# Optimization experiments

Measured on AMD Instinct MI355X. Metric: run time of the kernel, lower is better.

Reference implementation:

```python
import jax, jax.numpy as jnp
import numpy as np
import math

# Config (matches init_kwargs): ProphetNet-style ngram self-attention
T, B, E, H, NGRAM, NB, MAXD = 512, 4, 1024, 16, 2, 32, 128
HD = E // H
TGT = (1 + NGRAM) * T
NEG = -1e9


def _buckets(rel):
    # faithful numpy version of _relative_positions_bucket (bidirectional=False)
    n = np.maximum(-rel, 0)
    max_exact = NB // 2
    is_small = n < max_exact
    large = max_exact + np.log(np.maximum(n, 1) / max_exact) / math.log(MAXD / max_exact) * (NB - max_exact)
    large = np.minimum(large, NB - 1).astype(np.int32)
    return np.where(is_small, n.astype(np.int32), large)


def setup_inputs() -> dict:
    key = jax.random.key(0)
    ks = jax.random.split(key, 4)
    s = 0.02
    # position ids 1..T (ProphetNet positions start at 1); precompute bucket tables
    pos = np.arange(1, T + 1, dtype=np.int64)[None, :].repeat(B, axis=0)          # [B,T]
    main_rel = pos[:, None, :] - pos[:, :, None]                                  # [B,T,T]
    pred_keys = np.concatenate([pos - 1, pos], axis=-1)                           # [B,2T]
    pred_rel = pred_keys[:, None, :] - pos[:, :, None]                            # [B,T,2T]
    return {
        "query": jax.random.normal(ks[0], (TGT, B, E), jnp.float32),
        "in_proj_weight": jax.random.normal(ks[1], (3 * E, E), jnp.float32) * s,
        "in_proj_bias": jnp.zeros((3 * E,), jnp.float32),
        "rel_w": jax.random.normal(ks[2], (NB * H, E), jnp.float32) * s,
        "rel_b": jnp.zeros((NB * H,), jnp.float32),
        "out_w": jax.random.normal(ks[3], (E, E), jnp.float32) * s,
        "out_b": jnp.zeros((E,), jnp.float32),
        "main_buckets": jnp.asarray(_buckets(main_rel), jnp.int32),
        "predict_buckets": jnp.asarray(_buckets(pred_rel), jnp.int32),
    }


def reference(query, in_proj_weight, in_proj_bias, rel_w, rel_b, out_w, out_b,
              main_buckets, predict_buckets):
    scaling = HD ** -0.5
    qkv = query @ in_proj_weight.T + in_proj_bias                  # [TGT,B,3E]
    q, k, v = jnp.split(qkv, 3, axis=-1)
    q = q * scaling

    def heads(x):  # [TGT,B,E] -> [B*H, TGT, HD]
        return x.reshape(TGT, B * H, HD).transpose(1, 0, 2)

    q, k, v = heads(q), heads(k), heads(v)
    q_main, k_main, v_main = q[:, :T], k[:, :T], v[:, :T]

    def ngram_split(x):  # [B*H, NGRAM*T, HD] -> [N, B*H, T, HD]
        return x[:, T:].reshape(B * H, NGRAM, T, HD).transpose(1, 0, 2, 3)

    q_pred, k_pred, v_pred = ngram_split(q), ngram_split(k), ngram_split(v)
    h_main = query[:T]                                             # [T,B,E]
    h_pred = query[T:].reshape(NGRAM, T, B, E)

    # ---------- main stream ----------
    aw_main = jnp.einsum('bth,bsh->bts', q_main, k_main)           # [B*H,T,T]
    vals = h_main.transpose(1, 0, 2) @ rel_w.T + rel_b             # [B,T,NB*H]
    vals = vals.reshape(B, T, NB, H).transpose(0, 3, 1, 2)         # [B,H,T,NB]
    idx = jnp.broadcast_to(main_buckets[:, None], (B, H, T, T))
    rel_main = jnp.take_along_axis(vals, idx, axis=-1).reshape(B * H, T, T)
    causal = jnp.triu(jnp.full((T, T), NEG, jnp.float32), 1)       # self_attn_mask
    aw_main = jax.nn.softmax(aw_main + rel_main + causal[None], axis=-1)
    attn_main = jnp.einsum('bts,bsh->bth', aw_main, v_main)        # [B*H,T,HD]
    attn_main = attn_main.transpose(1, 0, 2).reshape(1, T, B, E)
    attn_main = attn_main @ out_w.T + out_b

    # ---------- ngram predict streams ----------
    k_ng = jnp.concatenate([jnp.broadcast_to(k_main[None], (NGRAM, B * H, T, HD)), k_pred], axis=2)
    v_ng = jnp.concatenate([jnp.broadcast_to(v_main[None], (NGRAM, B * H, T, HD)), v_pred], axis=2)
    aw_ng = jnp.einsum('nbtc,nbsc->nbts', q_pred, k_ng)            # [N,B*H,T,2T]
    valsn = h_pred.transpose(0, 2, 1, 3) @ rel_w.T + rel_b         # [N,B,T,NB*H]
    valsn = valsn.reshape(NGRAM, B, T, NB, H).transpose(0, 1, 4, 2, 3)  # [N,B,H,T,NB]
    idxn = jnp.broadcast_to(predict_buckets[None, :, None], (NGRAM, B, H, T, 2 * T))
    rel_ng = jnp.take_along_axis(valsn, idxn, axis=-1).reshape(NGRAM, B * H, T, 2 * T)
    # ngram_mask: main part causal, predict part only the matching position
    ng_mask = jnp.concatenate([causal, NEG * (1.0 - jnp.eye(T, dtype=jnp.float32))], axis=1)  # [T,2T]
    aw_ng = jax.nn.softmax(aw_ng + rel_ng + ng_mask[None, None], axis=-1)
    attn_ng = jnp.einsum('nbts,nbsc->nbtc', aw_ng, v_ng)           # [N,B*H,T,HD]
    attn_ng = attn_ng.transpose(0, 2, 1, 3).reshape(NGRAM, T, B, E)
    attn_ng = attn_ng @ out_w.T + out_b

    return jnp.concatenate([attn_main, attn_ng], axis=0).reshape(TGT, B, E)
```

## Files before the change

kernel.cpp:

```cpp
#include <hip/hip_runtime.h>
#include <hip/hip_bf16.h>
#include <math.h>

constexpr int T_ = 512;
constexpr int B_ = 4;
constexpr int E_ = 1024;
constexpr int H_ = 16;
constexpr int NGRAM_ = 2;
constexpr int TGT_ = (1 + NGRAM_) * T_;
constexpr int ROWS_ = TGT_ * B_;

typedef __bf16 bf16_t;
typedef __bf16 bf16x8 __attribute__((ext_vector_type(8)));
typedef __bf16 bf16x4 __attribute__((ext_vector_type(4)));
typedef float f32x4 __attribute__((ext_vector_type(4)));

#define GLL(gaddr, laddr)                                                     \
  __builtin_amdgcn_global_load_lds(                                           \
      (const __attribute__((address_space(1))) void*)(gaddr),                 \
      (__attribute__((address_space(3))) void*)(laddr), 16, 0, 0)

#define BARX()  asm volatile("s_barrier" ::: "memory")
#define WVM7()  asm volatile("s_waitcnt vmcnt(7)" ::: "memory")
#define WVM0()  asm volatile("s_waitcnt vmcnt(0)" ::: "memory")

__global__ __launch_bounds__(256) void prep(
    const float* __restrict__ query, const float* __restrict__ ipw,
    const float* __restrict__ relw, const float* __restrict__ outw,
    bf16_t* __restrict__ qb, bf16_t* __restrict__ ipwb,
    bf16_t* __restrict__ relwb, bf16_t* __restrict__ outwb) {
  const int i = blockIdx.x * 256 + threadIdx.x;
  constexpr int N1 = ROWS_ * E_ / 4;
  constexpr int N2 = 3 * E_ * E_ / 4;
  constexpr int N3 = 512 * E_ / 4;
  constexpr int N4 = E_ * E_ / 4;
  const float4* src;
  bf16_t* dst;
  int j = i;
  if (i < N1) { src = (const float4*)query; dst = qb; }
  else if (i < N1 + N2) { src = (const float4*)ipw; dst = ipwb; j = i - N1; }
  else if (i < N1 + N2 + N3) { src = (const float4*)relw; dst = relwb; j = i - N1 - N2; }
  else if (i < N1 + N2 + N3 + N4) { src = (const float4*)outw; dst = outwb; j = i - N1 - N2 - N3; }
  else return;
  const float4 v = src[j];
  bf16x4 o;
  o[0] = (bf16_t)v.x; o[1] = (bf16_t)v.y;
  o[2] = (bf16_t)v.z; o[3] = (bf16_t)v.w;
  ((bf16x4*)dst)[j] = o;
}

__device__ __forceinline__ int sw256(int row, int col) {
  return row * 256 + ((((col >> 3) ^ (row & 31)) << 3) | (col & 7));
}

__global__ __launch_bounds__(512, 2) void bgemm_proj(
    const bf16_t* __restrict__ A, const bf16_t* __restrict__ W,
    const float* __restrict__ ipb, const float* __restrict__ relb,
    bf16_t* __restrict__ qkvb, float* __restrict__ relv2,
    bf16_t* __restrict__ vT) {
  __shared__ bf16_t smem[57344];
  bf16_t* As0 = smem;
  bf16_t* As1 = smem + 12288;
  bf16_t* Bs0 = smem + 24576;
  bf16_t* Bs1 = smem + 24576 + 16384;

  const int tid = threadIdx.x;
  const int wave = tid >> 6, lane = tid & 63;
  const int wr = wave >> 2, wc = wave & 3;
  const int pid = blockIdx.y * 14 + blockIdx.x;
  const int lid = (pid & 7) * 56 + (pid >> 3);
  const int by = lid / 14;
  const int bx = lid - by * 14;
  const int bm = by * 192, bn = bx * 256;
  const int q = lane >> 4, ln = lane & 15;
  const int grow = tid >> 3;
  const int gcol = ((tid & 7) ^ (grow & 7)) * 8;
  const int co[2] = {((q) ^ (ln & 7)) * 8, ((4 + q) ^ (ln & 7)) * 8};

  f32x4 acc[6][4];
#pragma unroll
  for (int mi = 0; mi < 6; ++mi)
#pragma unroll
    for (int ni = 0; ni < 4; ++ni)
#pragma unroll
      for (int r = 0; r < 4; ++r) acc[mi][ni][r] = 0.f;

  auto stage = [&](int kt, bf16_t* la, bf16_t* lb) {
    const int kc = kt * 64 + gcol;
#pragma unroll
    for (int p = 0; p < 3; ++p)
      GLL(&A[(size_t)(bm + p * 64 + grow) * 1024 + kc], &la[p * 4096 + tid * 8]);
#pragma unroll
    for (int p = 0; p < 4; ++p)
      GLL(&W[(size_t)(bn + p * 64 + grow) * 1024 + kc], &lb[p * 4096 + tid * 8]);
  };

  auto compute_tile = [&](const bf16_t* la, const bf16_t* lb) {
    bf16x8 a0[3], a1[3], b0[4], b1[4];
#pragma unroll
    for (int ni = 0; ni < 4; ++ni)
      b0[ni] = *(const bf16x8*)&lb[(wc * 64 + ni * 16 + ln) * 64 + co[0]];
#pragma unroll
    for (int mi = 0; mi < 3; ++mi)
      a0[mi] = *(const bf16x8*)&la[(wr * 96 + mi * 16 + ln) * 64 + co[0]];
#pragma unroll
    for (int mi = 0; mi < 3; ++mi)
      a1[mi] = *(const bf16x8*)&la[(wr * 96 + (3 + mi) * 16 + ln) * 64 + co[0]];
    __builtin_amdgcn_s_setprio(1);
#pragma unroll
    for (int mi = 0; mi < 3; ++mi)
#pragma unroll
      for (int ni = 0; ni < 4; ++ni)
        acc[mi][ni] = __builtin_amdgcn_mfma_f32_16x16x32_bf16(
            a0[mi], b0[ni], acc[mi][ni], 0, 0, 0);
    __builtin_amdgcn_s_setprio(0);
#pragma unroll
    for (int ni = 0; ni < 4; ++ni)
      b1[ni] = *(const bf16x8*)&lb[(wc * 64 + ni * 16 + ln) * 64 + co[1]];
#pragma unroll
    for (int mi = 0; mi < 3; ++mi)
      a0[mi] = *(const bf16x8*)&la[(wr * 96 + mi * 16 + ln) * 64 + co[1]];
    __builtin_amdgcn_s_setprio(1);
#pragma unroll
    for (int mi = 0; mi < 3; ++mi)
#pragma unroll
      for (int ni = 0; ni < 4; ++ni)
        acc[3 + mi][ni] = __builtin_amdgcn_mfma_f32_16x16x32_bf16(
            a1[mi], b0[ni], acc[3 + mi][ni], 0, 0, 0);
    __builtin_amdgcn_s_setprio(0);
#pragma unroll
    for (int mi = 0; mi < 3; ++mi)
      a1[mi] = *(const bf16x8*)&la[(wr * 96 + (3 + mi) * 16 + ln) * 64 + co[1]];
    __builtin_amdgcn_s_setprio(1);
#pragma unroll
    for (int mi = 0; mi < 3; ++mi)
#pragma unroll
      for (int ni = 0; ni < 4; ++ni)
        acc[mi][ni] = __builtin_amdgcn_mfma_f32_16x16x32_bf16(
            a0[mi], b1[ni], acc[mi][ni], 0, 0, 0);
    __builtin_amdgcn_s_setprio(0);
    __builtin_amdgcn_s_setprio(1);
#pragma unroll
    for (int mi = 0; mi < 3; ++mi)
#pragma unroll
      for (int ni = 0; ni < 4; ++ni)
        acc[3 + mi][ni] = __builtin_amdgcn_mfma_f32_16x16x32_bf16(
            a1[mi], b1[ni], acc[3 + mi][ni], 0, 0, 0);
    __builtin_amdgcn_s_setprio(0);
  };

  stage(0, As0, Bs0);
  stage(1, As1, Bs1);

  for (int kt = 0; kt < 16; kt += 2) {
    WVM7(); BARX();
    compute_tile(As0, Bs0);
    BARX();
    if (kt + 2 < 16) stage(kt + 2, As0, Bs0);
    if (kt < 14) { WVM7(); } else { WVM0(); }
    BARX();
    compute_tile(As1, Bs1);
    BARX();
    if (kt + 3 < 16) stage(kt + 3, As1, Bs1);
  }

  if (bn < 2048) {
    const float sc = (bn < 1024) ? 0.125f : 1.0f;
#pragma unroll
    for (int mi = 0; mi < 6; ++mi) {
#pragma unroll
      for (int ni = 0; ni < 4; ++ni) {
        const int col = bn + wc * 64 + ni * 16 + ln;
        const float bv = ipb[col];
#pragma unroll
        for (int r = 0; r < 4; ++r) {
          const int row = bm + wr * 96 + mi * 16 + q * 4 + r;
          qkvb[(size_t)row * 3072 + col] = (bf16_t)((acc[mi][ni][r] + bv) * sc);
        }
      }
    }
  } else if (bn < 3072) {
    __syncthreads();
#pragma unroll
    for (int mi = 0; mi < 6; ++mi) {
#pragma unroll
      for (int ni = 0; ni < 4; ++ni) {
        const int col_l = wc * 64 + ni * 16 + ln;
        const float bv = ipb[bn + col_l];
#pragma unroll
        for (int r = 0; r < 4; ++r) {
          const int row_l = wr * 96 + mi * 16 + q * 4 + r;
          smem[sw256(row_l, col_l)] = (bf16_t)(acc[mi][ni][r] + bv);
        }
      }
    }
    __syncthreads();
    const int h0 = (bn - 2048) >> 6;
    const int tb0 = bm >> 2;
#pragma unroll
    for (int e = 0; e < 2; ++e) {
      const int task = e * 512 + tid;
      const int b = task & 3;
      const int c = task >> 2;
      const int h = h0 + (c >> 6);
      const int d = c & 63;
      const size_t base = ((size_t)((b * 16 + h) * 64 + d)) * (size_t)TGT_ + tb0;
#pragma unroll
      for (int k = 0; k < 6; ++k) {
        bf16x8 v8;
#pragma unroll
        for (int i = 0; i < 8; ++i)
          v8[i] = smem[sw256((k * 8 + i) * 4 + b, c)];
        *(bf16x8*)&vT[base + k * 8] = v8;
      }
    }
  } else {
    const int cb = bn - 3072 + wc * 64;
    float4 rb4;
#pragma unroll
    for (int ni = 0; ni < 4; ++ni)
      ((float*)&rb4)[ni] = relb[cb + ni * 16 + ln];
    const int bkbase = cb >> 4;
#pragma unroll
    for (int mi = 0; mi < 6; ++mi) {
#pragma unroll
      for (int r = 0; r < 4; ++r) {
        const int row = bm + wr * 96 + mi * 16 + q * 4 + r;
        float4 v;
        v.x = acc[mi][0][r] + rb4.x;
        v.y = acc[mi][1][r] + rb4.y;
        v.z = acc[mi][2][r] + rb4.z;
        v.w = acc[mi][3][r] + rb4.w;
        *(float4*)&relv2[(size_t)row * 512 + ln * 32 + bkbase] = v;
      }
    }
  }
}

__global__ __launch_bounds__(256, 4) void bgemm_out(
    const bf16_t* __restrict__ A, const bf16_t* __restrict__ W,
    const float* __restrict__ bias, float* __restrict__ C, int N) {
  __shared__ bf16_t As[128 * 64];
  __shared__ bf16_t Bs[128 * 64];

  const int tid = threadIdx.x;
  const int wave = tid >> 6, lane = tid & 63;
  const int wr = wave >> 1, wc = wave & 1;
  const int pid = blockIdx.y * 8 + blockIdx.x;
  const int lid = (pid & 7) * 48 + (pid >> 3);
  const int bm = (lid >> 3) * 128, bn = (lid & 7) * 128;
  const int q = lane >> 4, ln = lane & 15;
  const int grow = tid >> 3;
  const int gcol = ((tid & 7) ^ (grow & 7)) * 8;

  f32x4 acc[4][4];
#pragma unroll
  for (int mi = 0; mi < 4; ++mi)
#pragma unroll
    for (int ni = 0; ni < 4; ++ni)
#pragma unroll
      for (int r = 0; r < 4; ++r) acc[mi][ni][r] = 0.f;

  const int co[2] = {((q) ^ (ln & 7)) * 8, ((4 + q) ^ (ln & 7)) * 8};

  for (int k0 = 0; k0 < 1024; k0 += 64) {
    __syncthreads();
#pragma unroll
    for (int p = 0; p < 4; ++p) {
      GLL(&A[(size_t)(bm + p * 32 + grow) * 1024 + k0 + gcol], &As[p * 2048 + tid * 8]);
      GLL(&W[(size_t)(bn + p * 32 + grow) * 1024 + k0 + gcol], &Bs[p * 2048 + tid * 8]);
    }
    __syncthreads();
#pragma unroll
    for (int t = 0; t < 2; ++t) {
      bf16x8 af[4], bf[4];
#pragma unroll
      for (int mi = 0; mi < 4; ++mi)
        af[mi] = *(const bf16x8*)&As[(wr * 64 + mi * 16 + ln) * 64 + co[t]];
#pragma unroll
      for (int ni = 0; ni < 4; ++ni)
        bf[ni] = *(const bf16x8*)&Bs[(wc * 64 + ni * 16 + ln) * 64 + co[t]];
#pragma unroll
      for (int mi = 0; mi < 4; ++mi)
#pragma unroll
        for (int ni = 0; ni < 4; ++ni)
          acc[mi][ni] = __builtin_amdgcn_mfma_f32_16x16x32_bf16(
              af[mi], bf[ni], acc[mi][ni], 0, 0, 0);
    }
  }

#pragma unroll
  for (int mi = 0; mi < 4; ++mi) {
#pragma unroll
    for (int ni = 0; ni < 4; ++ni) {
      const int col = bn + wc * 64 + ni * 16 + ln;
      const float bv = bias[col];
#pragma unroll
      for (int r = 0; r < 4; ++r) {
        const int row = bm + wr * 64 + mi * 16 + q * 4 + r;
        C[(size_t)row * N + col] = acc[mi][ni][r] + bv;
      }
    }
  }
}

__device__ __forceinline__ int bucket_of(int n) {
  if (n < 16) return n;
  const float lf = __log2f((float)n);
  int b = (int)(16.0f + (lf - 4.0f) * 5.3333333f);
  return b > 31 ? 31 : b;
}

__global__ __launch_bounds__(256, 2) void flash_mfma(
    const bf16_t* __restrict__ qkvb, const bf16_t* __restrict__ vT,
    const float* __restrict__ relv2, bf16_t* __restrict__ attn) {
  __shared__ bf16_t Ks[2][64 * 64];
  __shared__ bf16_t Vts[2][64 * 64];
  __shared__ bf16_t Ps[4][16 * 64];
  __shared__ bf16_t biasS[3][64 * 33];

  const int bh = blockIdx.x;
  const int qt = 7 - ((blockIdx.y + (bh >> 3)) & 7);
  const int tq0 = qt * 64;
  const int b = bh >> 4, h = bh & 15;
  const int tid = threadIdx.x;
  const int wave = tid >> 6, lane = tid & 63;
  const int q = lane >> 4, ln = lane & 15;
  const int m0 = wave * 16;
  const int grow = tid >> 3;
  const int gcol = ((tid & 7) ^ (grow & 7)) * 8;
  const int co[2] = {((q) ^ (ln & 7)) * 8, ((4 + q) ^ (ln & 7)) * 8};

#pragma unroll
  for (int z = 0; z < 3; ++z) {
#pragma unroll
    for (int u = 0; u < 2; ++u) {
      const int c = u * 256 + tid;
      const int row = c >> 3, j4 = (c & 7) * 4;
      const float4 v = *(const float4*)
          &relv2[((size_t)(z * T_ + tq0 + row) * B_ + b) * 512 + h * 32 + j4];
      biasS[z][row * 33 + j4 + 0] = (bf16_t)v.x;
      biasS[z][row * 33 + j4 + 1] = (bf16_t)v.y;
      biasS[z][row * 33 + j4 + 2] = (bf16_t)v.z;
      biasS[z][row * 33 + j4 + 3] = (bf16_t)v.w;
    }
  }

#pragma unroll
  for (int u = 0; u < 2; ++u) {
    const int sr = u * 32 + grow;
    GLL(&qkvb[((size_t)(0 * T_ + tq0 + sr) * B_ + b) * 3072 + h * 64 + gcol],
        &Ks[0][u * 2048 + tid * 8]);
    GLL(&qkvb[((size_t)(1 * T_ + tq0 + sr) * B_ + b) * 3072 + h * 64 + gcol],
        &Vts[0][u * 2048 + tid * 8]);
    GLL(&qkvb[((size_t)(2 * T_ + tq0 + sr) * B_ + b) * 3072 + h * 64 + gcol],
        &Ks[1][u * 2048 + tid * 8]);
  }
  __syncthreads();

  bf16x8 aq[3][2];
  aq[0][0] = *(const bf16x8*)&Ks[0][(m0 + ln) * 64 + co[0]];
  aq[0][1] = *(const bf16x8*)&Ks[0][(m0 + ln) * 64 + co[1]];
  aq[1][0] = *(const bf16x8*)&Vts[0][(m0 + ln) * 64 + co[0]];
  aq[1][1] = *(const bf16x8*)&Vts[0][(m0 + ln) * 64 + co[1]];
  aq[2][0] = *(const bf16x8*)&Ks[1][(m0 + ln) * 64 + co[0]];
  aq[2][1] = *(const bf16x8*)&Ks[1][(m0 + ln) * 64 + co[1]];

  float bv31[3][4], bv0[3][4];
#pragma unroll
  for (int z = 0; z < 3; ++z)
#pragma unroll
    for (int r = 0; r < 4; ++r) {
      const int rloc = m0 + q * 4 + r;
      bv31[z][r] = (float)biasS[z][rloc * 33 + 31];
      bv0[z][r] = (float)biasS[z][rloc * 33];
    }

  f32x4 Od[3][4];
  float lpart[3][4];
#pragma unroll
  for (int z = 0; z < 3; ++z)
#pragma unroll
    for (int r = 0; r < 4; ++r) {
      lpart[z][r] = 0.f;
#pragma unroll
      for (int tc = 0; tc < 4; ++tc) Od[z][tc][r] = 0.f;
    }

  const int ntiles = qt + 3;

  auto stage_tile = [&](int jj, int buf) {
    const int krb = (jj <= qt) ? jj * 64 : ((jj - qt) * T_ + tq0);
#pragma unroll
    for (int u = 0; u < 2; ++u) {
      const int sr = u * 32 + grow;
      GLL(&qkvb[((size_t)(krb + sr) * B_ + b) * 3072 + 1024 + h * 64 + gcol],
          &Ks[buf][u * 2048 + tid * 8]);
      GLL(&vT[((size_t)bh * 64 + sr) * (size_t)TGT_ + krb + gcol],
          &Vts[buf][u * 2048 + tid * 8]);
    }
  };

  __syncthreads();
  stage_tile(0, 0);
  __syncthreads();

  for (int jj = 0; jj < ntiles; ++jj) {
    const int cur = jj & 1;
    if (jj + 1 < ntiles) stage_tile(jj + 1, cur ^ 1);

    const int krb = (jj <= qt) ? jj * 64 : ((jj - qt) * T_ + tq0);

    bf16x8 kf[4][2], vf[4][2];
#pragma unroll
    for (int tc = 0; tc < 4; ++tc) {
      kf[tc][0] = *(const bf16x8*)&Ks[cur][(tc * 16 + ln) * 64 + co[0]];
      kf[tc][1] = *(const bf16x8*)&Ks[cur][(tc * 16 + ln) * 64 + co[1]];
      vf[tc][0] = *(const bf16x8*)&Vts[cur][(tc * 16 + ln) * 64 + co[0]];
      vf[tc][1] = *(const bf16x8*)&Vts[cur][(tc * 16 + ln) * 64 + co[1]];
    }

    if (jj <= qt) {
      const bool far = (jj <= qt - 3);
#pragma unroll
      for (int z = 0; z < 3; ++z) {
        f32x4 acc[4];
#pragma unroll
        for (int tc = 0; tc < 4; ++tc)
#pragma unroll
          for (int r = 0; r < 4; ++r) acc[tc][r] = 0.f;
#pragma unroll
        for (int tc = 0; tc < 4; ++tc) {
          acc[tc] = __builtin_amdgcn_mfma_f32_16x16x32_bf16(aq[z][0], kf[tc][0], acc[tc], 0, 0, 0);
          acc[tc] = __builtin_amdgcn_mfma_f32_16x16x32_bf16(aq[z][1], kf[tc][1], acc[tc], 0, 0, 0);
        }

        if (far) {
#pragma unroll
          for (int r = 0; r < 4; ++r) {
            const float bv = bv31[z][r];
#pragma unroll
            for (int tc = 0; tc < 4; ++tc) {
              const float p = __expf(acc[tc][r] + bv);
              lpart[z][r] += p;
              const int pc = (tc * 2 + (ln >> 3)) ^ ((q * 4 + r) & 7);
              Ps[wave][(q * 4 + r) * 64 + pc * 8 + (ln & 7)] = (bf16_t)p;
            }
          }
        } else {
#pragma unroll
          for (int r = 0; r < 4; ++r) {
            const int rloc = m0 + q * 4 + r;
            const int dbase = tq0 + rloc - krb;
#pragma unroll
            for (int tc = 0; tc < 4; ++tc) {
              const int sl = tc * 16 + ln;
              const int d = dbase - sl;
              const bool valid = (jj < qt) | (d >= 0);
              int n = d < 0 ? 0 : d;
              if (z > 0) n += 1;
              const float bv = (float)biasS[z][rloc * 33 + bucket_of(n)];
              const float p = valid ? __expf(acc[tc][r] + bv) : 0.f;
              lpart[z][r] += p;
              const int pc = (tc * 2 + (ln >> 3)) ^ ((q * 4 + r) & 7);
              Ps[wave][(q * 4 + r) * 64 + pc * 8 + (ln & 7)] = (bf16_t)p;
            }
          }
        }

        bf16x8 ap[2];
        ap[0] = *(const bf16x8*)&Ps[wave][ln * 64 + co[0]];
        ap[1] = *(const bf16x8*)&Ps[wave][ln * 64 + co[1]];
#pragma unroll
        for (int tc = 0; tc < 4; ++tc) {
          Od[z][tc] = __builtin_amdgcn_mfma_f32_16x16x32_bf16(ap[0], vf[tc][0], Od[z][tc], 0, 0, 0);
          Od[z][tc] = __builtin_amdgcn_mfma_f32_16x16x32_bf16(ap[1], vf[tc][1], Od[z][tc], 0, 0, 0);
        }
      }
    } else {
#pragma unroll
      for (int z = 1; z <= 2; ++z) {
        if (jj - qt == z) {
          f32x4 acc[4];
#pragma unroll
          for (int tc = 0; tc < 4; ++tc)
#pragma unroll
            for (int r = 0; r < 4; ++r) acc[tc][r] = 0.f;
#pragma unroll
          for (int tc = 0; tc < 4; ++tc) {
            acc[tc] = __builtin_amdgcn_mfma_f32_16x16x32_bf16(aq[z][0], kf[tc][0], acc[tc], 0, 0, 0);
            acc[tc] = __builtin_amdgcn_mfma_f32_16x16x32_bf16(aq[z][1], kf[tc][1], acc[tc], 0, 0, 0);
          }
#pragma unroll
          for (int r = 0; r < 4; ++r) {
            const int rloc = m0 + q * 4 + r;
            const float bv = bv0[z][r];
#pragma unroll
            for (int tc = 0; tc < 4; ++tc) {
              const int sl = tc * 16 + ln;
              const float p = (sl == rloc) ? __expf(acc[tc][r] + bv) : 0.f;
              lpart[z][r] += p;
              const int pc = (tc * 2 + (ln >> 3)) ^ ((q * 4 + r) & 7);
              Ps[wave][(q * 4 + r) * 64 + pc * 8 + (ln & 7)] = (bf16_t)p;
            }
          }
          bf16x8 ap[2];
          ap[0] = *(const bf16x8*)&Ps[wave][ln * 64 + co[0]];
          ap[1] = *(const bf16x8*)&Ps[wave][ln * 64 + co[1]];
#pragma unroll
          for (int tc = 0; tc < 4; ++tc) {
            Od[z][tc] = __builtin_amdgcn_mfma_f32_16x16x32_bf16(ap[0], vf[tc][0], Od[z][tc], 0, 0, 0);
            Od[z][tc] = __builtin_amdgcn_mfma_f32_16x16x32_bf16(ap[1], vf[tc][1], Od[z][tc], 0, 0, 0);
          }
        }
      }
    }
    __syncthreads();
  }

#pragma unroll
  for (int z = 0; z < 3; ++z) {
#pragma unroll
    for (int r = 0; r < 4; ++r) {
      float l = lpart[z][r];
      l += __shfl_xor(l, 1, 16);
      l += __shfl_xor(l, 2, 16);
      l += __shfl_xor(l, 4, 16);
      l += __shfl_xor(l, 8, 16);
      const float inv = 1.f / l;
      const size_t rowbase =
          ((size_t)(z * T_ + tq0 + m0 + q * 4 + r) * B_ + b) * (size_t)E_ + h * 64;
#pragma unroll
      for (int tc = 0; tc < 4; ++tc)
        attn[rowbase + tc * 16 + ln] = (bf16_t)(Od[z][tc][r] * inv);
    }
  }
}

extern "C" void kernel_launch(void* const* d_in, const int* in_sizes, int n_in,
                              void* d_out, int out_size, void* d_ws, size_t ws_size,
                              hipStream_t stream) {
  const float* query = (const float*)d_in[0];
  const float* ipw   = (const float*)d_in[1];
  const float* ipb   = (const float*)d_in[2];
  const float* relw  = (const float*)d_in[3];
  const float* relb  = (const float*)d_in[4];
  const float* outw  = (const float*)d_in[5];
  const float* outb  = (const float*)d_in[6];
  float* out = (float*)d_out;

  bf16_t* qkvb  = (bf16_t*)d_ws;
  float*  relv2 = (float*)(qkvb + (size_t)ROWS_ * 3 * E_);
  bf16_t* qb    = (bf16_t*)(relv2 + (size_t)ROWS_ * 512);
  bf16_t* ipwb  = qb + (size_t)ROWS_ * E_;
  bf16_t* relwb = ipwb + (size_t)(3 * E_) * E_;
  bf16_t* outwb = relwb + (size_t)512 * E_;
  bf16_t* attnb = outwb + (size_t)E_ * E_;
  bf16_t* vT    = attnb + (size_t)ROWS_ * E_;

  const dim3 blk(256);

  {
    const int ntot = (ROWS_ * E_ + 3 * E_ * E_ + 512 * E_ + E_ * E_) / 4;
    prep<<<dim3((ntot + 255) / 256), blk, 0, stream>>>(
        query, ipw, relw, outw, qb, ipwb, relwb, outwb);
  }

  bgemm_proj<<<dim3(3584 / 256, ROWS_ / 192), dim3(512), 0, stream>>>(
      qb, ipwb, ipb, relb, qkvb, relv2, vT);

  flash_mfma<<<dim3(64, 8), blk, 0, stream>>>(
      qkvb, vT, relv2, attnb);

  bgemm_out<<<dim3(E_ / 128, ROWS_ / 128), blk, 0, stream>>>(
      attnb, outwb, outb, out, E_);
}
```

Measured before the change: 239.6 us.

## Double-buffer output GEMM with 192x128 tiles and split projection GEMM launch

```diff
diff --git a/kernel.cpp b/kernel.cpp
--- a/kernel.cpp
+++ b/kernel.cpp
@@ -20,9 +20,10 @@
       (const __attribute__((address_space(1))) void*)(gaddr),                 \
       (__attribute__((address_space(3))) void*)(laddr), 16, 0, 0)
 
-#define BARX()  asm volatile("s_barrier" ::: "memory")
-#define WVM7()  asm volatile("s_waitcnt vmcnt(7)" ::: "memory")
-#define WVM0()  asm volatile("s_waitcnt vmcnt(0)" ::: "memory")
+#define BARX()   asm volatile("s_barrier" ::: "memory")
+#define WVM7()   asm volatile("s_waitcnt vmcnt(7)" ::: "memory")
+#define WVM10()  asm volatile("s_waitcnt vmcnt(10)" ::: "memory")
+#define WVM0()   asm volatile("s_waitcnt vmcnt(0)" ::: "memory")
 
 __global__ __launch_bounds__(256) void prep(
     const float* __restrict__ query, const float* __restrict__ ipw,
@@ -57,7 +58,7 @@
     const bf16_t* __restrict__ A, const bf16_t* __restrict__ W,
     const float* __restrict__ ipb, const float* __restrict__ relb,
     bf16_t* __restrict__ qkvb, float* __restrict__ relv2,
-    bf16_t* __restrict__ vT) {
+    bf16_t* __restrict__ vT, int bn0) {
   __shared__ bf16_t smem[57344];
   bf16_t* As0 = smem;
   bf16_t* As1 = smem + 12288;
@@ -67,11 +68,13 @@
   const int tid = threadIdx.x;
   const int wave = tid >> 6, lane = tid & 63;
   const int wr = wave >> 2, wc = wave & 3;
-  const int pid = blockIdx.y * 14 + blockIdx.x;
-  const int lid = (pid & 7) * 56 + (pid >> 3);
-  const int by = lid / 14;
-  const int bx = lid - by * 14;
-  const int bm = by * 192, bn = bx * 256;
+  const int nx = gridDim.x;
+  const int pid = blockIdx.y * nx + blockIdx.x;
+  const int chunk = (nx * gridDim.y) >> 3;
+  const int lid = (pid & 7) * chunk + (pid >> 3);
+  const int by = lid / nx;
+  const int bx = lid - by * nx;
+  const int bm = by * 192, bn = bn0 + bx * 256;
   const int q = lane >> 4, ln = lane & 15;
   const int grow = tid >> 3;
   const int gcol = ((tid & 7) ^ (grow & 7)) * 8;
@@ -237,68 +240,123 @@
   }
 }
 
-__global__ __launch_bounds__(256, 4) void bgemm_out(
+__global__ __launch_bounds__(256, 1) void bgemm_out(
     const bf16_t* __restrict__ A, const bf16_t* __restrict__ W,
-    const float* __restrict__ bias, float* __restrict__ C, int N) {
-  __shared__ bf16_t As[128 * 64];
-  __shared__ bf16_t Bs[128 * 64];
+    const float* __restrict__ bias, float* __restrict__ C) {
+  __shared__ bf16_t smem[40960];
 
   const int tid = threadIdx.x;
   const int wave = tid >> 6, lane = tid & 63;
   const int wr = wave >> 1, wc = wave & 1;
   const int pid = blockIdx.y * 8 + blockIdx.x;
-  const int lid = (pid & 7) * 48 + (pid >> 3);
-  const int bm = (lid >> 3) * 128, bn = (lid & 7) * 128;
+  const int lid = (pid & 7) * 32 + (pid >> 3);
+  const int bm = (lid >> 3) * 192, bn = (lid & 7) * 128;
   const int q = lane >> 4, ln = lane & 15;
   const int grow = tid >> 3;
   const int gcol = ((tid & 7) ^ (grow & 7)) * 8;
-
-  f32x4 acc[4][4];
-#pragma unroll
-  for (int mi = 0; mi < 4; ++mi)
+  const int co[2] = {((q) ^ (ln & 7)) * 8, ((4 + q) ^ (ln & 7)) * 8};
+
+  f32x4 acc[6][4];
+#pragma unroll
+  for (int mi = 0; mi < 6; ++mi)
 #pragma unroll
     for (int ni = 0; ni < 4; ++ni)
 #pragma unroll
       for (int r = 0; r < 4; ++r) acc[mi][ni][r] = 0.f;
 
-  const int co[2] = {((q) ^ (ln & 7)) * 8, ((4 + q) ^ (ln & 7)) * 8};
-
-  for (int k0 = 0; k0 < 1024; k0 += 64) {
-    __syncthreads();
-#pragma unroll
-    for (int p = 0; p < 4; ++p) {
-      GLL(&A[(size_t)(bm + p * 32 + grow) * 1024 + k0 + gcol], &As[p * 2048 + tid * 8]);
-      GLL(&W[(size_t)(bn + p * 32 + grow) * 1024 + k0 + gcol], &Bs[p * 2048 + tid * 8]);
-    }
-    __syncthreads();
-#pragma unroll
-    for (int t = 0; t < 2; ++t) {
-      bf16x8 af[4], bf[4];
-#pragma unroll
-      for (int mi = 0; mi < 4; ++mi)
-        af[mi] = *(const bf16x8*)&As[(wr * 64 + mi * 16 + ln) * 64 + co[t]];
-#pragma unroll
-      for (int ni = 0; ni < 4; ++ni)
-        bf[ni] = *(const bf16x8*)&Bs[(wc * 64 + ni * 16 + ln) * 64 + co[t]];
-#pragma unroll
-      for (int mi = 0; mi < 4; ++mi)
-#pragma unroll
-        for (int ni = 0; ni < 4; ++ni)
-          acc[mi][ni] = __builtin_amdgcn_mfma_f32_16x16x32_bf16(
-              af[mi], bf[ni], acc[mi][ni], 0, 0, 0);
-    }
-  }
-
-#pragma unroll
-  for (int mi = 0; mi < 4; ++mi) {
+  auto stage = [&](int kt) {
+    bf16_t* s = smem + (kt & 1) * 20480;
+    const int kc = kt * 64 + gcol;
+#pragma unroll
+    for (int p = 0; p < 6; ++p)
+      GLL(&A[(size_t)(bm + p * 32 + grow) * 1024 + kc], &s[p * 2048 + tid * 8]);
+#pragma unroll
+    for (int p = 0; p < 4; ++p)
+      GLL(&W[(size_t)(bn + p * 32 + grow) * 1024 + kc],
+          &s[12288 + p * 2048 + tid * 8]);
+  };
+
+  auto compute_tile = [&](int kt) {
+    const bf16_t* la = smem + (kt & 1) * 20480;
+    const bf16_t* lb = la + 12288;
+    bf16x8 a0[3], a1[3], b0[4], b1[4];
+#pragma unroll
+    for (int ni = 0; ni < 4; ++ni)
+      b0[ni] = *(const bf16x8*)&lb[(wc * 64 + ni * 16 + ln) * 64 + co[0]];
+#pragma unroll
+    for (int mi = 0; mi < 3; ++mi)
+      a0[mi] = *(const bf16x8*)&la[(wr * 96 + mi * 16 + ln) * 64 + co[0]];
+#pragma unroll
+    for (int mi = 0; mi < 3; ++mi)
+      a1[mi] = *(const bf16x8*)&la[(wr * 96 + (3 + mi) * 16 + ln) * 64 + co[0]];
+    __builtin_amdgcn_s_setprio(1);
+#pragma unroll
+    for (int mi = 0; mi < 3; ++mi)
+#pragma unroll
+      for (int ni = 0; ni < 4; ++ni)
+        acc[mi][ni] = __builtin_amdgcn_mfma_f32_16x16x32_bf16(
+            a0[mi], b0[ni], acc[mi][ni], 0, 0, 0);
+    __builtin_amdgcn_s_setprio(0);
+#pragma unroll
+    for (int ni = 0; ni < 4; ++ni)
+      b1[ni] = *(const bf16x8*)&lb[(wc * 64 + ni * 16 + ln) * 64 + co[1]];
+#pragma unroll
+    for (int mi = 0; mi < 3; ++mi)
+      a0[mi] = *(const bf16x8*)&la[(wr * 96 + mi * 16 + ln) * 64 + co[1]];
+    __builtin_amdgcn_s_setprio(1);
+#pragma unroll
+    for (int mi = 0; mi < 3; ++mi)
+#pragma unroll
+      for (int ni = 0; ni < 4; ++ni)
+        acc[3 + mi][ni] = __builtin_amdgcn_mfma_f32_16x16x32_bf16(
+            a1[mi], b0[ni], acc[3 + mi][ni], 0, 0, 0);
+    __builtin_amdgcn_s_setprio(0);
+#pragma unroll
+    for (int mi = 0; mi < 3; ++mi)
+      a1[mi] = *(const bf16x8*)&la[(wr * 96 + (3 + mi) * 16 + ln) * 64 + co[1]];
+    __builtin_amdgcn_s_setprio(1);
+#pragma unroll
+    for (int mi = 0; mi < 3; ++mi)
+#pragma unroll
+      for (int ni = 0; ni < 4; ++ni)
+        acc[mi][ni] = __builtin_amdgcn_mfma_f32_16x16x32_bf16(
+            a0[mi], b1[ni], acc[mi][ni], 0, 0, 0);
+    __builtin_amdgcn_s_setprio(0);
+    __builtin_amdgcn_s_setprio(1);
+#pragma unroll
+    for (int mi = 0; mi < 3; ++mi)
+#pragma unroll
+      for (int ni = 0; ni < 4; ++ni)
+        acc[3 + mi][ni] = __builtin_amdgcn_mfma_f32_16x16x32_bf16(
+            a1[mi], b1[ni], acc[3 + mi][ni], 0, 0, 0);
+    __builtin_amdgcn_s_setprio(0);
+  };
+
+  stage(0);
+  stage(1);
+
+  for (int kt = 0; kt < 16; kt += 2) {
+    WVM10(); BARX();
+    compute_tile(kt);
+    BARX();
+    if (kt + 2 < 16) stage(kt + 2);
+    if (kt < 14) { WVM10(); } else { WVM0(); }
+    BARX();
+    compute_tile(kt + 1);
+    BARX();
+    if (kt + 3 < 16) stage(kt + 3);
+  }
+
+#pragma unroll
+  for (int mi = 0; mi < 6; ++mi) {
 #pragma unroll
     for (int ni = 0; ni < 4; ++ni) {
       const int col = bn + wc * 64 + ni * 16 + ln;
       const float bv = bias[col];
 #pragma unroll
       for (int r = 0; r < 4; ++r) {
-        const int row = bm + wr * 64 + mi * 16 + q * 4 + r;
-        C[(size_t)row * N + col] = acc[mi][ni][r] + bv;
+        const int row = bm + wr * 96 + mi * 16 + q * 4 + r;
+        C[(size_t)row * 1024 + col] = acc[mi][ni][r] + bv;
       }
     }
   }
@@ -566,12 +624,14 @@
         query, ipw, relw, outw, qb, ipwb, relwb, outwb);
   }
 
-  bgemm_proj<<<dim3(3584 / 256, ROWS_ / 192), dim3(512), 0, stream>>>(
-      qb, ipwb, ipb, relb, qkvb, relv2, vT);
+  bgemm_proj<<<dim3(8, 32), dim3(512), 0, stream>>>(
+      qb, ipwb, ipb, relb, qkvb, relv2, vT, 0);
+  bgemm_proj<<<dim3(6, 32), dim3(512), 0, stream>>>(
+      qb, ipwb, ipb, relb, qkvb, relv2, vT, 2048);
 
   flash_mfma<<<dim3(64, 8), blk, 0, stream>>>(
       qkvb, vT, relv2, attnb);
 
-  bgemm_out<<<dim3(E_ / 128, ROWS_ / 128), blk, 0, stream>>>(
-      attnb, outwb, outb, out, E_);
+  bgemm_out<<<dim3(8, 32), blk, 0, stream>>>(
+      attnb, outwb, outb, out);
 }
```

New measurement: 242.0 us. Within noise of the previous version (+1.0%).
